# Optimization experiments

Measured on AMD Instinct MI355X. Metric: run time of the kernel, lower is better.

Reference implementation:

```python
import jax, jax.numpy as jnp
import numpy as np

DIM = 512
DIM_INPUTS = (8,)*4 + (16,)*4 + (32,)*4 + (64,)*4 + (128,)*4 + (256,)*4  # 24 bands, sum=2016
N_BANDS = len(DIM_INPUTS)
TOTAL_OUT2 = 2 * sum(DIM_INPUTS)  # 4032 (concatenated last-layer gated width)
B, T = 4, 512


def _glu_tanh(z):
    # LinearGLUWithTanH epilogue: chunk last dim, tanh(a) * sigmoid(gate)
    a, gate = jnp.split(z, 2, axis=-1)
    return jnp.tanh(a) * jax.nn.sigmoid(gate)


def setup_inputs() -> dict:
    key = jax.random.key(0)
    k0, k1, k2, k3, k4 = jax.random.split(key, 5)
    x = jax.random.normal(k0, (B, T, N_BANDS, DIM), dtype=jnp.float32)
    # layer 0: per-band Linear(DIM, 2*DIM), stacked over bands
    W0 = jax.random.normal(k1, (N_BANDS, DIM, 2 * DIM), dtype=jnp.float32) / np.float32(np.sqrt(DIM))
    b0 = jax.random.normal(k2, (N_BANDS, 2 * DIM), dtype=jnp.float32) * 0.01
    # layer 1 (last): per-band Linear(DIM, 2*dim_in); widths differ, so pack
    # all bands' weight columns into one concatenated matrix sliced statically.
    W1 = jax.random.normal(k3, (DIM, TOTAL_OUT2), dtype=jnp.float32) / np.float32(np.sqrt(DIM))
    b1 = jax.random.normal(k4, (TOTAL_OUT2,), dtype=jnp.float32) * 0.01
    return {"x": x, "W0": W0, "b0": b0, "W1": W1, "b1": b1}


def reference(x, W0, b0, W1, b1):
    # layer 0 for all bands in one grouped GEMM: (b t n d),(n d e)->(b t n e)
    h = _glu_tanh(jnp.einsum('btnd,nde->btne', x, W0) + b0)  # (B,T,N,DIM)
    outs = []
    off = 0
    for i, di in enumerate(DIM_INPUTS):  # static loop over structurally distinct bands
        w = W1[:, off:off + 2 * di]
        bb = b1[off:off + 2 * di]
        outs.append(_glu_tanh(h[:, :, i] @ w + bb))  # (B,T,di)
        off += 2 * di
    return jnp.concatenate(outs, axis=-1)  # (B,T,sum(DIM_INPUTS))
```

## Files before the change

kernel.cpp:

```cpp
#include <hip/hip_runtime.h>
#include <cstdint>
#include <cstddef>


typedef _Float16 f16;
typedef _Float16 f16x8 __attribute__((ext_vector_type(8)));
typedef float floatx4 __attribute__((ext_vector_type(4)));

#define BT 2048
#define NB 24

__device__ __forceinline__ int band_di(int b){ return 8 << (b >> 2); }
__device__ __forceinline__ int band_off2(int b){
  int g = b >> 2;
  return 2 * (32 * ((1 << g) - 1) + (b & 3) * (8 << g));
}

__device__ __forceinline__ float fsigm(float x){
  return __builtin_amdgcn_rcpf(1.f + __expf(-x));
}
__device__ __forceinline__ float ftanh(float x){
  return 1.f - 2.f * __builtin_amdgcn_rcpf(1.f + __expf(2.f * x));
}

__device__ __forceinline__ void gl_lds16(const void* g, void* l){
  __builtin_amdgcn_global_load_lds(
      (const __attribute__((address_space(1))) unsigned int*)g,
      (__attribute__((address_space(3))) unsigned int*)l, 16, 0, 0);
}


__global__ __launch_bounds__(256) void cast_x(const float4* __restrict__ in,
                                              f16* __restrict__ out){
  int t = blockIdx.x * 256 + threadIdx.x;
  float4 v = in[t];
  f16 o0 = (f16)v.x, o1 = (f16)v.y, o2 = (f16)v.z, o3 = (f16)v.w;
  typedef _Float16 f16x4 __attribute__((ext_vector_type(4)));
  f16x4 o = { o0, o1, o2, o3 };
  *(f16x4*)(out + (size_t)t * 4) = o;
}

__global__ __launch_bounds__(256) void cast_w0(const float* __restrict__ W0,
                                               f16* __restrict__ w0t){
  __shared__ float tile[64][33];
  int bid = blockIdx.x;
  int dt   = bid & 7;
  int half = (bid >> 3) & 1;
  int g    = (bid >> 4) & 15;
  int band = bid >> 8;
  int t = threadIdx.x;
  int c0 = half * 512 + g * 32;
  int d0 = dt * 64;
  int r  = t >> 2;
  int cs = (t & 3) * 8;
  const float* src = W0 + ((size_t)(band * 512 + d0 + r)) * 1024 + c0 + cs;
  float4 v0 = *(const float4*)src;
  float4 v1 = *(const float4*)(src + 4);
  tile[r][cs + 0] = v0.x; tile[r][cs + 1] = v0.y; tile[r][cs + 2] = v0.z; tile[r][cs + 3] = v0.w;
  tile[r][cs + 4] = v1.x; tile[r][cs + 5] = v1.y; tile[r][cs + 6] = v1.z; tile[r][cs + 7] = v1.w;
  __syncthreads();
  int i   = t >> 3;
  int ds8 = (t & 7) * 8;
  int prow = g * 64 + 2 * i + half;
  f16x8 o;
  #pragma unroll
  for (int k = 0; k < 8; ++k) o[k] = (f16)tile[ds8 + k][i];
  *(f16x8*)(w0t + ((size_t)(band * 1024 + prow)) * 512 + d0 + ds8) = o;
}

__global__ __launch_bounds__(256) void cast_w1(const float* __restrict__ W1,
                                               f16* __restrict__ w1t){
  int t = blockIdx.x * 256 + threadIdx.x;
  int j  = t >> 6;
  int d8 = (t & 63) * 8;
  int band = 23;
  for (int b = 0; b < 24; ++b){ if (j < band_off2(b + 1)) { band = b; break; } }
  int off2 = band_off2(band);
  int di = band_di(band);
  int p = j - off2;
  int oc = off2 + ((p & 1) ? di + (p >> 1) : (p >> 1));
  f16x8 o;
  #pragma unroll
  for (int k = 0; k < 8; ++k) o[k] = (f16)W1[(size_t)(d8 + k) * 4032 + oc];
  *(f16x8*)(w1t + (size_t)j * 512 + d8) = o;
}

__global__ __launch_bounds__(256) void cast_bias(const float* __restrict__ b0,
                                                 const float* __restrict__ b1,
                                                 float* __restrict__ b0p,
                                                 float* __restrict__ b1p){
  int t = blockIdx.x * 256 + threadIdx.x;
  if (t < NB * 1024){
    int p = t & 1023;
    int base = t & ~1023;
    b0p[t] = b0[base + ((p & 1) ? 512 + (p >> 1) : (p >> 1))];
  } else {
    int j = t - NB * 1024;
    if (j < 4032){
      int band = 23;
      for (int b = 0; b < 24; ++b){ if (j < band_off2(b + 1)) { band = b; break; } }
      int off2 = band_off2(band);
      int di = band_di(band);
      int p = j - off2;
      b1p[j] = b1[off2 + ((p & 1) ? di + (p >> 1) : (p >> 1))];
    }
  }
}

__global__ __launch_bounds__(256) void gemm1(const f16* __restrict__ xh,
                                             const f16* __restrict__ w0t,
                                             const float* __restrict__ b0p,
                                             f16* __restrict__ h){
  __shared__ __align__(16) f16 As[128 * 64];
  __shared__ __align__(16) f16 Bs[128 * 64];
  int bid = blockIdx.x;
  int nt = bid & 7;
  int mt = (bid >> 3) & 15;
  int band = bid >> 7;
  int t = threadIdx.x;
  int lane = t & 63, w = t >> 6;
  int wm = w & 1, wn = w >> 1;
  int quad = lane >> 4, lc = lane & 15;
  floatx4 acc[4][4];
  #pragma unroll
  for (int i = 0; i < 4; ++i)
    #pragma unroll
    for (int j = 0; j < 4; ++j) acc[i][j] = floatx4{0.f, 0.f, 0.f, 0.f};

  const int mrow0 = mt * 128;
  const int nrow0 = nt * 128;
  for (int kb = 0; kb < 8; ++kb){
    const int k0 = kb * 64;
    #pragma unroll
    for (int p = 0; p < 4; ++p){
      int idx = p * 256 + t;
      int r = idx >> 3, s = idx & 7;
      int l = s ^ (r & 7);
      gl_lds16(xh + ((size_t)(mrow0 + r) * 24 + band) * 512 + k0 + l * 8,
               &As[idx * 8]);
    }
    #pragma unroll
    for (int p = 0; p < 4; ++p){
      int idx = p * 256 + t;
      int r = idx >> 3, s = idx & 7;
      int l = s ^ (r & 7);
      gl_lds16(w0t + ((size_t)(band * 1024 + nrow0 + r)) * 512 + k0 + l * 8,
               &Bs[idx * 8]);
    }
    __syncthreads();
    #pragma unroll
    for (int s2 = 0; s2 < 2; ++s2){
      int kc = s2 * 4 + quad;
      f16x8 af[4], bf[4];
      #pragma unroll
      for (int i = 0; i < 4; ++i){
        int m = wm * 64 + i * 16 + lc;
        af[i] = *(const f16x8*)&As[m * 64 + ((kc ^ (m & 7)) << 3)];
        int n = wn * 64 + i * 16 + lc;
        bf[i] = *(const f16x8*)&Bs[n * 64 + ((kc ^ (n & 7)) << 3)];
      }
      #pragma unroll
      for (int i = 0; i < 4; ++i)
        #pragma unroll
        for (int j = 0; j < 4; ++j)
          acc[i][j] = __builtin_amdgcn_mfma_f32_16x16x32_f16(af[i], bf[j], acc[i][j], 0, 0, 0);
    }
    __syncthreads();
  }
  #pragma unroll
  for (int j = 0; j < 4; ++j){
    int colp = nrow0 + wn * 64 + j * 16 + lc;
    float bias = b0p[band * 1024 + colp];
    #pragma unroll
    for (int i = 0; i < 4; ++i){
      int mbase = mrow0 + wm * 64 + i * 16 + quad * 4;
      #pragma unroll
      for (int r = 0; r < 4; ++r){
        float z = acc[i][j][r] + bias;
        float zp = __shfl_xor(z, 1);
        if (!(lc & 1)){
          float hv = ftanh(z) * fsigm(zp);
          h[((size_t)band * BT + mbase + r) * 512 + (colp >> 1)] = (f16)hv;
        }
      }
    }
  }
}

template<int BN>
__device__ __forceinline__ void gemm2_tile(const f16* __restrict__ hb,
                                           const f16* __restrict__ w1t,
                                           const float* __restrict__ b1p,
                                           float* __restrict__ out,
                                           int band, int mt, int ntile,
                                           f16* As, f16* Bs){
  constexpr int WNW = (BN == 128) ? 2 : 1;
  constexpr int WMW = 4 / WNW;
  constexpr int MF = 128 / (WMW * 16);
  constexpr int NF = BN / (WNW * 16);
  int t = threadIdx.x;
  int lane = t & 63, w = t >> 6;
  int wm = (WNW == 2) ? (w & 1) : w;
  int wn = (WNW == 2) ? (w >> 1) : 0;
  int quad = lane >> 4, lc = lane & 15;
  int off2 = band_off2(band);
  int jbase = off2 + ntile * BN;
  floatx4 acc[MF][NF];
  #pragma unroll
  for (int i = 0; i < MF; ++i)
    #pragma unroll
    for (int j = 0; j < NF; ++j) acc[i][j] = floatx4{0.f, 0.f, 0.f, 0.f};

  for (int kb = 0; kb < 8; ++kb){
    int k0 = kb * 64;
    #pragma unroll
    for (int p = 0; p < 4; ++p){
      int idx = p * 256 + t;
      int r = idx >> 3, s = idx & 7, l = s ^ (r & 7);
      gl_lds16(hb + ((size_t)(mt * 128 + r)) * 512 + k0 + l * 8, &As[idx * 8]);
    }
    constexpr int BCH = BN * 8;
    constexpr int BP = (BCH + 255) / 256;
    #pragma unroll
    for (int p = 0; p < BP; ++p){
      int idx = p * 256 + t;
      if ((BCH % 256 == 0) || idx < BCH){
        int r = idx >> 3, s = idx & 7, l = s ^ (r & 7);
        gl_lds16(w1t + ((size_t)(jbase + r)) * 512 + k0 + l * 8, &Bs[idx * 8]);
      }
    }
    __syncthreads();
    #pragma unroll
    for (int s2 = 0; s2 < 2; ++s2){
      int kc = s2 * 4 + quad;
      f16x8 af[MF], bf[NF];
      #pragma unroll
      for (int i = 0; i < MF; ++i){
        int m = wm * (MF * 16) + i * 16 + lc;
        af[i] = *(const f16x8*)&As[m * 64 + ((kc ^ (m & 7)) << 3)];
      }
      #pragma unroll
      for (int j = 0; j < NF; ++j){
        int n = wn * (NF * 16) + j * 16 + lc;
        bf[j] = *(const f16x8*)&Bs[n * 64 + ((kc ^ (n & 7)) << 3)];
      }
      #pragma unroll
      for (int i = 0; i < MF; ++i)
        #pragma unroll
        for (int j = 0; j < NF; ++j)
          acc[i][j] = __builtin_amdgcn_mfma_f32_16x16x32_f16(af[i], bf[j], acc[i][j], 0, 0, 0);
    }
    __syncthreads();
  }
  int outbase = off2 >> 1;
  #pragma unroll
  for (int j = 0; j < NF; ++j){
    int p = ntile * BN + wn * (NF * 16) + j * 16 + lc;
    float bias = b1p[off2 + p];
    #pragma unroll
    for (int i = 0; i < MF; ++i){
      int mbase = mt * 128 + wm * (MF * 16) + i * 16 + quad * 4;
      #pragma unroll
      for (int r = 0; r < 4; ++r){
        float z = acc[i][j][r] + bias;
        float zp = __shfl_xor(z, 1);
        if (!(lc & 1)){
          out[(size_t)(mbase + r) * 2016 + outbase + (p >> 1)] = ftanh(z) * fsigm(zp);
        }
      }
    }
  }
}

__global__ __launch_bounds__(256) void gemm2(const f16* __restrict__ h,
                                             const f16* __restrict__ w1t,
                                             const float* __restrict__ b1p,
                                             float* __restrict__ out){
  __shared__ __align__(16) f16 As[128 * 64];
  __shared__ __align__(16) f16 Bs[128 * 64];
  int bid = blockIdx.x;
  int band, mt, ntile, cls;
  if (bid < 256){
    band = bid >> 4; mt = bid & 15; ntile = 0; cls = band >> 2;
  } else if (bid < 384){
    int rel = bid - 256; band = 16 + (rel >> 5);
    int r2 = rel & 31; mt = r2 & 15; ntile = r2 >> 4; cls = 4;
  } else {
    int rel = bid - 384; band = 20 + (rel >> 6);
    int r2 = rel & 63; mt = r2 & 15; ntile = r2 >> 4; cls = 5;
  }
  const f16* hb = h + ((size_t)band << 20);
  switch (cls){
    case 0:  gemm2_tile<16 >(hb, w1t, b1p, out, band, mt, ntile, As, Bs); break;
    case 1:  gemm2_tile<32 >(hb, w1t, b1p, out, band, mt, ntile, As, Bs); break;
    case 2:  gemm2_tile<64 >(hb, w1t, b1p, out, band, mt, ntile, As, Bs); break;
    default: gemm2_tile<128>(hb, w1t, b1p, out, band, mt, ntile, As, Bs); break;
  }
}

extern "C" void kernel_launch(void* const* d_in, const int* in_sizes, int n_in,
                              void* d_out, int out_size, void* d_ws, size_t ws_size,
                              hipStream_t stream){
  const float* x  = (const float*)d_in[0];
  const float* W0 = (const float*)d_in[1];
  const float* b0 = (const float*)d_in[2];
  const float* W1 = (const float*)d_in[3];
  const float* b1 = (const float*)d_in[4];
  char* ws = (char*)d_ws;
  f16*   xh   = (f16*)(ws);
  f16*   hbuf = (f16*)(ws + 50331648);
  f16*   w0t  = (f16*)(ws + 100663296);
  f16*   w1t  = (f16*)(ws + 125829120);
  float* b0p  = (float*)(ws + 129957888);
  float* b1p  = (float*)(ws + 130056192);

  cast_x   <<<24576, 256, 0, stream>>>((const float4*)x, xh);
  cast_w0  <<<6144,  256, 0, stream>>>(W0, w0t);
  cast_w1  <<<1008,  256, 0, stream>>>(W1, w1t);
  cast_bias<<<112,   256, 0, stream>>>(b0, b1, b0p, b1p);
  gemm1    <<<3072,  256, 0, stream>>>(xh, w0t, b0p, hbuf);
  gemm2    <<<640,   256, 0, stream>>>(hbuf, w1t, b1p, (float*)d_out);
}
```

Baseline: 341.4 us.

## Tile cast_w1 through LDS, precompute GEMM addresses, remap gemm1 block order

cast_w1 now handles 16 output rows per block. It reads W1 rows with coalesced float4 loads, transposes them through a shared-memory tile, and writes full 16-byte chunks, replacing scattered 4-byte strided gathers. Both GEMM kernels compute their global and LDS address pointers and swizzled fragment offsets once before the K loop, then step pointers by a fixed amount, which removes per-iteration integer index arithmetic. gemm1 also remaps block IDs so that consecutive blocks come from different bands and tiles, likely to spread work across XCDs and caches, which may change L2 reuse of shared A and B tiles.

New measurement: 317.6 us. 1.07x faster.

```diff
diff --git a/kernel.cpp b/kernel.cpp
--- a/kernel.cpp
+++ b/kernel.cpp
@@ -34,9 +34,8 @@
                                               f16* __restrict__ out){
   int t = blockIdx.x * 256 + threadIdx.x;
   float4 v = in[t];
-  f16 o0 = (f16)v.x, o1 = (f16)v.y, o2 = (f16)v.z, o3 = (f16)v.w;
   typedef _Float16 f16x4 __attribute__((ext_vector_type(4)));
-  f16x4 o = { o0, o1, o2, o3 };
+  f16x4 o = { (f16)v.x, (f16)v.y, (f16)v.z, (f16)v.w };
   *(f16x4*)(out + (size_t)t * 4) = o;
 }
 
@@ -70,19 +69,40 @@
 
 __global__ __launch_bounds__(256) void cast_w1(const float* __restrict__ W1,
                                                f16* __restrict__ w1t){
-  int t = blockIdx.x * 256 + threadIdx.x;
-  int j  = t >> 6;
-  int d8 = (t & 63) * 8;
+  __shared__ f16 tile[16][520];
+  int jt = blockIdx.x;
+  int j16 = jt * 16;
   int band = 23;
-  for (int b = 0; b < 24; ++b){ if (j < band_off2(b + 1)) { band = b; break; } }
-  int off2 = band_off2(band);
-  int di = band_di(band);
-  int p = j - off2;
-  int oc = off2 + ((p & 1) ? di + (p >> 1) : (p >> 1));
-  f16x8 o;
-  #pragma unroll
-  for (int k = 0; k < 8; ++k) o[k] = (f16)W1[(size_t)(d8 + k) * 4032 + oc];
-  *(f16x8*)(w1t + (size_t)j * 512 + d8) = o;
+  for (int b = 0; b < 24; ++b){ if (j16 < band_off2(b + 1)) { band = b; break; } }
+  int off2 = band_off2(band), di = band_di(band);
+  int p0 = j16 - off2;
+  int oca = off2 + (p0 >> 1);
+  int ocg = oca + di;
+  int t = threadIdx.x;
+  #pragma unroll
+  for (int hh = 0; hh < 2; ++hh){
+    int d = hh * 256 + t;
+    const float* rowp = W1 + (size_t)d * 4032;
+    float4 a0 = *(const float4*)(rowp + oca);
+    float4 a1 = *(const float4*)(rowp + oca + 4);
+    float4 g0 = *(const float4*)(rowp + ocg);
+    float4 g1 = *(const float4*)(rowp + ocg + 4);
+    float av[8] = {a0.x,a0.y,a0.z,a0.w,a1.x,a1.y,a1.z,a1.w};
+    float gv[8] = {g0.x,g0.y,g0.z,g0.w,g1.x,g1.y,g1.z,g1.w};
+    #pragma unroll
+    for (int q = 0; q < 8; ++q){
+      tile[2*q][d]   = (f16)av[q];
+      tile[2*q+1][d] = (f16)gv[q];
+    }
+  }
+  __syncthreads();
+  int j = t & 15, dc = (t >> 4) * 32;
+  f16x8 o[4];
+  #pragma unroll
+  for (int k = 0; k < 4; ++k) o[k] = *(const f16x8*)&tile[j][dc + k*8];
+  f16* dst = w1t + (size_t)(j16 + j) * 512 + dc;
+  #pragma unroll
+  for (int k = 0; k < 4; ++k) *(f16x8*)(dst + k*8) = o[k];
 }
 
 __global__ __launch_bounds__(256) void cast_bias(const float* __restrict__ b0,
@@ -114,50 +134,58 @@
   __shared__ __align__(16) f16 As[128 * 64];
   __shared__ __align__(16) f16 Bs[128 * 64];
   int bid = blockIdx.x;
-  int nt = bid & 7;
-  int mt = (bid >> 3) & 15;
-  int band = bid >> 7;
+  int wid = (bid & 7) * 384 + (bid >> 3);
+  int band = wid >> 7;
+  int mt = (wid >> 3) & 15;
+  int nt = wid & 7;
   int t = threadIdx.x;
   int lane = t & 63, w = t >> 6;
   int wm = w & 1, wn = w >> 1;
   int quad = lane >> 4, lc = lane & 15;
-  floatx4 acc[4][4];
-  #pragma unroll
-  for (int i = 0; i < 4; ++i)
-    #pragma unroll
-    for (int j = 0; j < 4; ++j) acc[i][j] = floatx4{0.f, 0.f, 0.f, 0.f};
-
   const int mrow0 = mt * 128;
   const int nrow0 = nt * 128;
+
+  const char* gA[4]; const char* gB[4];
+  f16* lA[4]; f16* lB[4];
+  #pragma unroll
+  for (int p = 0; p < 4; ++p){
+    int idx = p * 256 + t;
+    int r = idx >> 3, s = idx & 7, l = s ^ (r & 7);
+    gA[p] = (const char*)(xh + ((size_t)(mrow0 + r) * 24 + band) * 512 + l * 8);
+    gB[p] = (const char*)(w0t + ((size_t)(band * 1024 + nrow0 + r)) * 512 + l * 8);
+    lA[p] = &As[idx * 8];
+    lB[p] = &Bs[idx * 8];
+  }
+  int aoff[4], boff[4];
+  #pragma unroll
+  for (int i = 0; i < 4; ++i){
+    int m = wm * 64 + i * 16 + lc;
+    aoff[i] = (m * 64 + ((quad ^ (m & 7)) << 3)) * 2;
+    int n = wn * 64 + i * 16 + lc;
+    boff[i] = (n * 64 + ((quad ^ (n & 7)) << 3)) * 2;
+  }
+  const char* Ab = (const char*)As;
+  const char* Bb = (const char*)Bs;
+
+  floatx4 acc[4][4];
+  #pragma unroll
+  for (int i = 0; i < 4; ++i)
+    #pragma unroll
+    for (int j = 0; j < 4; ++j) acc[i][j] = floatx4{0.f, 0.f, 0.f, 0.f};
+
   for (int kb = 0; kb < 8; ++kb){
-    const int k0 = kb * 64;
-    #pragma unroll
-    for (int p = 0; p < 4; ++p){
-      int idx = p * 256 + t;
-      int r = idx >> 3, s = idx & 7;
-      int l = s ^ (r & 7);
-      gl_lds16(xh + ((size_t)(mrow0 + r) * 24 + band) * 512 + k0 + l * 8,
-               &As[idx * 8]);
-    }
-    #pragma unroll
-    for (int p = 0; p < 4; ++p){
-      int idx = p * 256 + t;
-      int r = idx >> 3, s = idx & 7;
-      int l = s ^ (r & 7);
-      gl_lds16(w0t + ((size_t)(band * 1024 + nrow0 + r)) * 512 + k0 + l * 8,
-               &Bs[idx * 8]);
-    }
+    #pragma unroll
+    for (int p = 0; p < 4; ++p){ gl_lds16(gA[p], lA[p]); gA[p] += 128; }
+    #pragma unroll
+    for (int p = 0; p < 4; ++p){ gl_lds16(gB[p], lB[p]); gB[p] += 128; }
     __syncthreads();
     #pragma unroll
     for (int s2 = 0; s2 < 2; ++s2){
-      int kc = s2 * 4 + quad;
       f16x8 af[4], bf[4];
       #pragma unroll
       for (int i = 0; i < 4; ++i){
-        int m = wm * 64 + i * 16 + lc;
-        af[i] = *(const f16x8*)&As[m * 64 + ((kc ^ (m & 7)) << 3)];
-        int n = wn * 64 + i * 16 + lc;
-        bf[i] = *(const f16x8*)&Bs[n * 64 + ((kc ^ (n & 7)) << 3)];
+        af[i] = *(const f16x8*)(Ab + (aoff[i] ^ (s2 * 64)));
+        bf[i] = *(const f16x8*)(Bb + (boff[i] ^ (s2 * 64)));
       }
       #pragma unroll
       for (int i = 0; i < 4; ++i)
@@ -205,6 +233,39 @@
   int quad = lane >> 4, lc = lane & 15;
   int off2 = band_off2(band);
   int jbase = off2 + ntile * BN;
+
+  constexpr int BCH = BN * 8;
+  constexpr int BP = (BCH + 255) / 256;
+  const char* gA[4]; const char* gB[BP];
+  f16* lA[4]; f16* lB[BP];
+  #pragma unroll
+  for (int p = 0; p < 4; ++p){
+    int idx = p * 256 + t;
+    int r = idx >> 3, s = idx & 7, l = s ^ (r & 7);
+    gA[p] = (const char*)(hb + ((size_t)(mt * 128 + r)) * 512 + l * 8);
+    lA[p] = &As[idx * 8];
+  }
+  #pragma unroll
+  for (int p = 0; p < BP; ++p){
+    int idx = p * 256 + t;
+    int r = idx >> 3, s = idx & 7, l = s ^ (r & 7);
+    gB[p] = (const char*)(w1t + ((size_t)(jbase + r)) * 512 + l * 8);
+    lB[p] = &Bs[idx * 8];
+  }
+  int aoff[MF], boff[NF];
+  #pragma unroll
+  for (int i = 0; i < MF; ++i){
+    int m = wm * (MF * 16) + i * 16 + lc;
+    aoff[i] = (m * 64 + ((quad ^ (m & 7)) << 3)) * 2;
+  }
+  #pragma unroll
+  for (int j = 0; j < NF; ++j){
+    int n = wn * (NF * 16) + j * 16 + lc;
+    boff[j] = (n * 64 + ((quad ^ (n & 7)) << 3)) * 2;
+  }
+  const char* Ab = (const char*)As;
+  const char* Bb = (const char*)Bs;
+
   floatx4 acc[MF][NF];
   #pragma unroll
   for (int i = 0; i < MF; ++i)
@@ -212,38 +273,24 @@
     for (int j = 0; j < NF; ++j) acc[i][j] = floatx4{0.f, 0.f, 0.f, 0.f};
 
   for (int kb = 0; kb < 8; ++kb){
-    int k0 = kb * 64;
-    #pragma unroll
-    for (int p = 0; p < 4; ++p){
-      int idx = p * 256 + t;
-      int r = idx >> 3, s = idx & 7, l = s ^ (r & 7);
-      gl_lds16(hb + ((size_t)(mt * 128 + r)) * 512 + k0 + l * 8, &As[idx * 8]);
-    }
-    constexpr int BCH = BN * 8;
-    constexpr int BP = (BCH + 255) / 256;
+    #pragma unroll
+    for (int p = 0; p < 4; ++p){ gl_lds16(gA[p], lA[p]); gA[p] += 128; }
     #pragma unroll
     for (int p = 0; p < BP; ++p){
-      int idx = p * 256 + t;
-      if ((BCH % 256 == 0) || idx < BCH){
-        int r = idx >> 3, s = idx & 7, l = s ^ (r & 7);
-        gl_lds16(w1t + ((size_t)(jbase + r)) * 512 + k0 + l * 8, &Bs[idx * 8]);
+      if ((BCH % 256 == 0) || (p * 256 + t) < BCH){
+        gl_lds16(gB[p], lB[p]); gB[p] += 128;
       }
     }
     __syncthreads();
     #pragma unroll
     for (int s2 = 0; s2 < 2; ++s2){
-      int kc = s2 * 4 + quad;
       f16x8 af[MF], bf[NF];
       #pragma unroll
-      for (int i = 0; i < MF; ++i){
-        int m = wm * (MF * 16) + i * 16 + lc;
-        af[i] = *(const f16x8*)&As[m * 64 + ((kc ^ (m & 7)) << 3)];
-      }
-      #pragma unroll
-      for (int j = 0; j < NF; ++j){
-        int n = wn * (NF * 16) + j * 16 + lc;
-        bf[j] = *(const f16x8*)&Bs[n * 64 + ((kc ^ (n & 7)) << 3)];
-      }
+      for (int i = 0; i < MF; ++i)
+        af[i] = *(const f16x8*)(Ab + (aoff[i] ^ (s2 * 64)));
+      #pragma unroll
+      for (int j = 0; j < NF; ++j)
+        bf[j] = *(const f16x8*)(Bb + (boff[j] ^ (s2 * 64)));
       #pragma unroll
       for (int i = 0; i < MF; ++i)
         #pragma unroll
@@ -316,7 +363,7 @@
 
   cast_x   <<<24576, 256, 0, stream>>>((const float4*)x, xh);
   cast_w0  <<<6144,  256, 0, stream>>>(W0, w0t);
-  cast_w1  <<<1008,  256, 0, stream>>>(W1, w1t);
+  cast_w1  <<<252,   256, 0, stream>>>(W1, w1t);
   cast_bias<<<112,   256, 0, stream>>>(b0, b1, b0p, b1p);
   gemm1    <<<3072,  256, 0, stream>>>(xh, w0t, b0p, hbuf);
   gemm2    <<<640,   256, 0, stream>>>(hbuf, w1t, b1p, (float*)d_out);
```
